# Kernel optimization log

Hardware: AMD Instinct MI355X
Metric: run time of the kernel (lower is better)

Reference implementation:

```python
import jax, jax.numpy as jnp
import numpy as np

B, N, D, H, O = 8, 2048, 64, 64, 64
ALPHA = 2.0  # LeakyReLU negative slope per module default
NEG = -9e15


def _lin(x, W, b):
    # torch nn.Linear: y = x @ W.T + b, W is [out, in]
    return x @ W.T + b


def setup_inputs() -> dict:
    key = jax.random.key(0)
    ks = jax.random.split(key, 32)
    f32 = jnp.float32
    x = jax.random.normal(ks[0], (B, N, D), f32)
    adj = jax.random.randint(ks[1], (B, N, N), 0, 2).astype(f32)
    c = jax.random.normal(ks[2], (B, N, H), f32)
    h = jax.random.normal(ks[3], (B, N, H), f32)
    s = 0.1
    W = jax.random.normal(ks[4], (D, H), f32) * s           # GAT weight
    a = jax.random.normal(ks[5], (2 * H, 1), f32) * s       # GAT attention vector
    def lin(k, out_d, in_d):
        k1, k2 = jax.random.split(k)
        return (jax.random.normal(k1, (out_d, in_d), f32) * s,
                jax.random.normal(k2, (out_d,), f32) * s)
    Wf, bWf = lin(ks[6], H, H); Wi, bWi = lin(ks[7], H, H)
    Wo, bWo = lin(ks[8], H, H); Wc, bWc = lin(ks[9], H, H)
    Uf, bUf = lin(ks[10], H, D); Ui, bUi = lin(ks[11], H, D)
    Uo, bUo = lin(ks[12], H, D); Uc, bUc = lin(ks[13], H, D)
    Wout, bout = lin(ks[14], O, 2 * H)
    return dict(x=x, adj=adj, c=c, h=h, W=W, a=a,
                Wf=Wf, bWf=bWf, Wi=Wi, bWi=bWi, Wo=Wo, bWo=bWo, Wc=Wc, bWc=bWc,
                Uf=Uf, bUf=bUf, Ui=Ui, bUi=bUi, Uo=Uo, bUo=bUo, Uc=Uc, bUc=bUc,
                Wout=Wout, bout=bout)


def reference(x, adj, c, h, W, a,
              Wf, bWf, Wi, bWi, Wo, bWo, Wc, bWc,
              Uf, bUf, Ui, bUi, Uo, bUo, Uc, bUc,
              Wout, bout):
    # ---- GraphAttentionLayer (eval mode: dropout is identity) ----
    Wh = x @ W                                   # [B,N,H]
    # e[b,i,j] = leakyrelu(a[:H].Wh_i + a[H:].Wh_j) -- same math as the
    a_src = (Wh @ a[:H]).squeeze(-1)             # [B,N]
    a_dst = (Wh @ a[H:]).squeeze(-1)             # [B,N]
    e = jax.nn.leaky_relu(a_src[:, :, None] + a_dst[:, None, :], ALPHA)  # [B,N,N]
    att = jnp.where(adj > 0, e, NEG)
    att = jax.nn.softmax(att, axis=2)
    x_hidden = jax.nn.elu(att @ Wh)              # [B,N,H] (concat=True)
    # ---- LSTMLayer step ----
    f_t = jax.nn.sigmoid(_lin(h, Wf, bWf) + _lin(x, Uf, bUf))
    i_t = jax.nn.sigmoid(_lin(h, Wi, bWi) + _lin(x, Ui, bUi))
    o_t = jax.nn.sigmoid(_lin(h, Wo, bWo) + _lin(x, Uo, bUo))
    c_hat = jnp.tanh(_lin(h, Wc, bWc) + _lin(x, Uc, bUc))
    c_t = f_t * c + i_t * c_hat
    h_t = o_t * jax.nn.relu(c_t)                 # gate = nn.ReLU() default
    total = jnp.concatenate([x_hidden, h_t], axis=2)  # [B,N,2H]
    output = jax.nn.relu(_lin(total, Wout, bout))     # [B,N,O]
    return (output, h_t, c_t)
```

## Files before the change

kernel.cpp:

```cpp
#include <hip/hip_runtime.h>
#include <math.h>

#define B_ 8
#define N_ 2048
#define NT_ (B_*N_)
#define OUTSZ (NT_*64)

#define WS_ASRC  0
#define WS_ADST  (WS_ASRC + NT_)
#define WS_EJ    (WS_ADST + NT_)
#define WS_C1    (WS_EJ + NT_)
#define WS_C2    (WS_C1 + NT_)
#define WS_THR   (WS_C2 + NT_)
#define WS_GMAX  (WS_THR + NT_)
#define WS_WT    (WS_GMAX + 32)
#define WS_BB    (WS_WT + 128*256)
#define WS_WOT   (WS_BB + 256)
#define WS_PD    (WS_WOT + 128*64)
#define WS_PN    (WS_PD + 8*NT_)

typedef float f32x4 __attribute__((ext_vector_type(4)));
typedef __bf16 bf16x8 __attribute__((ext_vector_type(8)));
typedef __bf16 bf16x4 __attribute__((ext_vector_type(4)));

__device__ __forceinline__ float lrelu2(float x) { return x > 0.f ? x : 2.f * x; }
__device__ __forceinline__ float f4get(const float4& v, int k) { return k==0?v.x:(k==1?v.y:(k==2?v.z:v.w)); }

__global__ void k0_prep(const float* Wf, const float* Wi, const float* Wo, const float* Wc,
                        const float* Uf, const float* Ui, const float* Uo, const float* Uc,
                        const float* bWf, const float* bWi, const float* bWo, const float* bWc,
                        const float* bUf, const float* bUi, const float* bUo, const float* bUc,
                        const float* Wout, float* ws)
{
    int idx = blockIdx.x * 256 + threadIdx.x;
    if (idx < 128 * 256) {
        int k = idx >> 8, o = idx & 255;
        int g = o >> 6, u = o & 63;
        const float* Wg = (g == 0) ? Wf : (g == 1) ? Wi : (g == 2) ? Wo : Wc;
        const float* Ug = (g == 0) ? Uf : (g == 1) ? Ui : (g == 2) ? Uo : Uc;
        ws[WS_WT + idx] = (k < 64) ? Wg[u * 64 + k] : Ug[u * 64 + (k - 64)];
    } else if (idx < 128 * 256 + 256) {
        int o = idx - 128 * 256;
        int g = o >> 6, u = o & 63;
        const float* bW = (g == 0) ? bWf : (g == 1) ? bWi : (g == 2) ? bWo : bWc;
        const float* bU = (g == 0) ? bUf : (g == 1) ? bUi : (g == 2) ? bUo : bUc;
        ws[WS_BB + o] = bW[u] + bU[u];
    } else if (idx < 128 * 256 + 256 + 128 * 64) {
        int j = idx - (128 * 256 + 256);
        int k = j >> 6, u = j & 63;
        ws[WS_WOT + j] = Wout[u * 128 + k];
    }
}

__global__ __launch_bounds__(256) void k1_wh(const float* __restrict__ x, const float* __restrict__ W,
                                             const float* __restrict__ a, float* __restrict__ ws,
                                             __bf16* __restrict__ whT)
{
    __shared__ float xl[64 * 68];
    __shared__ float Wl[64 * 68];
    int t = threadIdx.x;
    int i0 = blockIdx.x * 64;
    #pragma unroll
    for (int it = 0; it < 4; ++it) {
        int f = t + 256 * it;
        int r = f >> 4, q = f & 15;
        *(float4*)&xl[r * 68 + q * 4] = *(const float4*)&x[i0 * 64 + f * 4];
        *(float4*)&Wl[r * 68 + q * 4] = *(const float4*)&W[f * 4];
    }
    __syncthreads();
    int cg = t & 15, rg = t >> 4;
    int c0 = cg * 4, r0 = rg * 4;
    float acc[4][4] = {};
    #pragma unroll
    for (int d0 = 0; d0 < 64; d0 += 4) {
        float4 wv[4], xv[4];
        #pragma unroll
        for (int k = 0; k < 4; ++k) wv[k] = *(float4*)&Wl[(d0 + k) * 68 + c0];
        #pragma unroll
        for (int ri = 0; ri < 4; ++ri) xv[ri] = *(float4*)&xl[(r0 + ri) * 68 + d0];
        #pragma unroll
        for (int ri = 0; ri < 4; ++ri)
            #pragma unroll
            for (int k = 0; k < 4; ++k) {
                float xs = f4get(xv[ri], k);
                acc[ri][0] += xs * wv[k].x; acc[ri][1] += xs * wv[k].y;
                acc[ri][2] += xs * wv[k].z; acc[ri][3] += xs * wv[k].w;
            }
    }
    int b = i0 >> 11;
    int rowb0 = (i0 & 2047) + r0;
    #pragma unroll
    for (int cj = 0; cj < 4; ++cj) {
        bf16x4 v;
        v[0] = (__bf16)acc[0][cj]; v[1] = (__bf16)acc[1][cj];
        v[2] = (__bf16)acc[2][cj]; v[3] = (__bf16)acc[3][cj];
        *(bf16x4*)&whT[((size_t)(b * 64 + c0 + cj)) * N_ + rowb0] = v;
    }
    float4 a0 = *(const float4*)&a[c0];
    float4 a1 = *(const float4*)&a[64 + c0];
    #pragma unroll
    for (int ri = 0; ri < 4; ++ri) {
        int row = i0 + r0 + ri;
        float s0 = acc[ri][0]*a0.x + acc[ri][1]*a0.y + acc[ri][2]*a0.z + acc[ri][3]*a0.w;
        float s1 = acc[ri][0]*a1.x + acc[ri][1]*a1.y + acc[ri][2]*a1.z + acc[ri][3]*a1.w;
        #pragma unroll
        for (int m = 1; m < 16; m <<= 1) { s0 += __shfl_xor(s0, m, 64); s1 += __shfl_xor(s1, m, 64); }
        if (cg == 0) { ws[WS_ASRC + row] = s0; ws[WS_ADST + row] = s1; }
    }
}

__global__ __launch_bounds__(256) void k1b_prep(float* ws)
{
    __shared__ float red[256];
    __shared__ float gsh;
    int b = blockIdx.x, t = threadIdx.x;
    float m = -3.0e38f;
    for (int j = t; j < N_; j += 256) {
        float v = ws[WS_ADST + b * N_ + j];
        ws[WS_EJ + b * N_ + j] = __expf(v);
        m = fmaxf(m, v);
    }
    red[t] = m; __syncthreads();
    for (int s = 128; s > 0; s >>= 1) { if (t < s) red[t] = fmaxf(red[t], red[t + s]); __syncthreads(); }
    if (t == 0) { gsh = red[0]; ws[WS_GMAX + b] = red[0]; }
    __syncthreads();
    float gmax = gsh;
    for (int i = t; i < N_; i += 256) {
        float as = ws[WS_ASRC + b * N_ + i];
        float M = lrelu2(as + gmax);
        ws[WS_C1 + b * N_ + i]  = __expf(as - M);
        ws[WS_C2 + b * N_ + i]  = __expf(2.f * as - M);
        ws[WS_THR + b * N_ + i] = __expf(-as);
    }
}

__global__ __launch_bounds__(256) void k2v3(const float* __restrict__ adj,
                                            const __bf16* __restrict__ whT,
                                            float* __restrict__ ws)
{
    __shared__ float lsa[4][16][68];
    __shared__ float lsd[4][16];
    int tid = threadIdx.x;
    int lane = tid & 63, w = tid >> 6;
    int r = lane & 15, g = lane >> 4;
    int jr = blockIdx.x & 7;
    int rblk = blockIdx.x >> 3;
    int b = rblk >> 4;
    int row_base = b * N_ + (rblk & 15) * 128;
    int jbeg = jr * 256 + w * 64;

    bf16x8 bfr[2][4];
    #pragma unroll
    for (int ks = 0; ks < 2; ++ks)
        #pragma unroll
        for (int n = 0; n < 4; ++n)
            bfr[ks][n] = *(const bf16x8*)&whT[(size_t)(b * 64 + n * 16 + r) * N_ + jbeg + ks * 32 + g * 8];
    float ejr[2][8];
    #pragma unroll
    for (int ks = 0; ks < 2; ++ks) {
        float4 e0 = *(const float4*)&ws[WS_EJ + b * N_ + jbeg + ks * 32 + g * 8];
        float4 e1 = *(const float4*)&ws[WS_EJ + b * N_ + jbeg + ks * 32 + g * 8 + 4];
        ejr[ks][0]=e0.x; ejr[ks][1]=e0.y; ejr[ks][2]=e0.z; ejr[ks][3]=e0.w;
        ejr[ks][4]=e1.x; ejr[ks][5]=e1.y; ejr[ks][6]=e1.z; ejr[ks][7]=e1.w;
    }

#define LDTILE(T, A0, A1, A2, A3, C1v, C2v, THv)                                   \
    {                                                                              \
        int row0_ = row_base + (T) * 16;                                           \
        const float* ap_ = &adj[(size_t)(row0_ + r) * N_ + jbeg];                  \
        A0 = *(const float4*)&ap_[g * 8];                                          \
        A1 = *(const float4*)&ap_[g * 8 + 4];                                      \
        A2 = *(const float4*)&ap_[32 + g * 8];                                     \
        A3 = *(const float4*)&ap_[32 + g * 8 + 4];                                 \
        C1v = ws[WS_C1 + row0_ + r];                                               \
        C2v = ws[WS_C2 + row0_ + r];                                               \
        THv = ws[WS_THR + row0_ + r];                                              \
    }

    float4 av0, av1, av2, av3; float c1, c2, thr;
    LDTILE(0, av0, av1, av2, av3, c1, c2, thr);

    for (int t = 0; t < 8; ++t) {
        int row0 = row_base + t * 16;
        f32x4 acc[4] = {{0.f,0.f,0.f,0.f},{0.f,0.f,0.f,0.f},{0.f,0.f,0.f,0.f},{0.f,0.f,0.f,0.f}};
        float dsum = 0.f;
        #pragma unroll
        for (int ks = 0; ks < 2; ++ks) {
            bf16x8 af;
            float ds_ = 0.f;
            #pragma unroll
            for (int e = 0; e < 8; ++e) {
                float avv = f4get(e < 4 ? (ks ? av2 : av0) : (ks ? av3 : av1), e & 3);
                float E = ejr[ks][e];
                float p = (E > thr) ? c1 * E : (c2 * E) * E;
                p = (avv > 0.f) ? p : 0.f;
                ds_ += p;
                af[e] = (__bf16)p;
            }
            dsum += ds_;
            #pragma unroll
            for (int n = 0; n < 4; ++n)
                acc[n] = __builtin_amdgcn_mfma_f32_16x16x32_bf16(af, bfr[ks][n], acc[n], 0, 0, 0);
        }
        float4 nv0, nv1, nv2, nv3; float n1, n2, n3;
        if (t < 7) { LDTILE(t + 1, nv0, nv1, nv2, nv3, n1, n2, n3); }
        dsum += __shfl_xor(dsum, 16, 64);
        dsum += __shfl_xor(dsum, 32, 64);
        #pragma unroll
        for (int n = 0; n < 4; ++n)
            #pragma unroll
            for (int i = 0; i < 4; ++i)
                lsa[w][g * 4 + i][n * 16 + r] = acc[n][i];
        if (g == 0) lsd[w][r] = dsum;
        __syncthreads();
        {
            int rl = tid >> 4, h0 = (tid & 15) * 4;
            float4 s = make_float4(0.f, 0.f, 0.f, 0.f);
            #pragma unroll
            for (int w2 = 0; w2 < 4; ++w2) {
                float4 q = *(const float4*)&lsa[w2][rl][h0];
                s.x += q.x; s.y += q.y; s.z += q.z; s.w += q.w;
            }
            *(float4*)&ws[WS_PN + ((size_t)jr * NT_ + row0 + rl) * 64 + h0] = s;
            if (tid < 16)
                ws[WS_PD + jr * NT_ + row0 + tid] = lsd[0][tid] + lsd[1][tid] + lsd[2][tid] + lsd[3][tid];
        }
        __syncthreads();
        av0 = nv0; av1 = nv1; av2 = nv2; av3 = nv3; c1 = n1; c2 = n2; thr = n3;
    }
#undef LDTILE
}

__global__ __launch_bounds__(256) void k3_lstm(const float* __restrict__ x, const float* __restrict__ c,
                                               const float* __restrict__ h, const float* __restrict__ ws,
                                               float* __restrict__ out)
{
    __shared__ float Al[16 * 132];
    __shared__ float gl[16 * 260];
    int t = threadIdx.x;
    int base = blockIdx.x * 16;
    {
        int r = t >> 4, k0 = (t & 15) * 8;
        const float* src = (k0 < 64) ? &h[(base + r) * 64 + k0] : &x[(base + r) * 64 + (k0 - 64)];
        *(float4*)&Al[r * 132 + k0]     = *(const float4*)&src[0];
        *(float4*)&Al[r * 132 + k0 + 4] = *(const float4*)&src[4];
    }
    __syncthreads();
    int og = t & 63, rg = t >> 6;
    int o0 = og * 4;
    const float* WT = &ws[WS_WT];
    float acc[4][4] = {};
    #pragma unroll
    for (int k0 = 0; k0 < 128; k0 += 4) {
        float4 wv[4], av[4];
        #pragma unroll
        for (int kk = 0; kk < 4; ++kk) wv[kk] = *(const float4*)&WT[(k0 + kk) * 256 + o0];
        #pragma unroll
        for (int rr = 0; rr < 4; ++rr) av[rr] = *(float4*)&Al[(rg + 4 * rr) * 132 + k0];
        #pragma unroll
        for (int rr = 0; rr < 4; ++rr)
            #pragma unroll
            for (int kk = 0; kk < 4; ++kk) {
                float as = f4get(av[rr], kk);
                acc[rr][0] += as * wv[kk].x; acc[rr][1] += as * wv[kk].y;
                acc[rr][2] += as * wv[kk].z; acc[rr][3] += as * wv[kk].w;
            }
    }
    float4 bbv = *(const float4*)&ws[WS_BB + o0];
    #pragma unroll
    for (int rr = 0; rr < 4; ++rr) {
        int r = rg + 4 * rr;
        *(float4*)&gl[r * 260 + o0] = make_float4(acc[rr][0] + bbv.x, acc[rr][1] + bbv.y,
                                                  acc[rr][2] + bbv.z, acc[rr][3] + bbv.w);
    }
    __syncthreads();
    int u = t & 63, rq = t >> 6;
    #pragma unroll
    for (int pp = 0; pp < 4; ++pp) {
        int r = rq + 4 * pp;
        float gf = gl[r * 260 + u];
        float gi = gl[r * 260 + 64 + u];
        float go = gl[r * 260 + 128 + u];
        float gc = gl[r * 260 + 192 + u];
        float fg = 1.f / (1.f + __expf(-gf));
        float ig = 1.f / (1.f + __expf(-gi));
        float oo = 1.f / (1.f + __expf(-go));
        float ch = tanhf(gc);
        float cv = c[(base + r) * 64 + u];
        float ct = fg * cv + ig * ch;
        float ht = oo * fmaxf(ct, 0.f);
        out[OUTSZ + (base + r) * 64 + u] = ht;
        out[2 * OUTSZ + (base + r) * 64 + u] = ct;
    }
}

__global__ __launch_bounds__(256) void k5_out(const float* __restrict__ ws, const float* __restrict__ bout,
                                              float* __restrict__ out)
{
    __shared__ float Al[64 * 132];
    int t = threadIdx.x;
    int base = blockIdx.x * 64;
    const float* ht = &out[OUTSZ];
    #pragma unroll
    for (int it = 0; it < 8; ++it) {
        int f = t + 256 * it;
        int r = f >> 5, q = f & 31;
        int k0 = q * 4;
        int row = base + r;
        float4 v;
        if (k0 < 64) {
            float4 s = make_float4(0.f, 0.f, 0.f, 0.f);
            float d = 0.f;
            #pragma unroll
            for (int jr = 0; jr < 8; ++jr) {
                float4 p = *(const float4*)&ws[WS_PN + ((size_t)jr * NT_ + row) * 64 + k0];
                s.x += p.x; s.y += p.y; s.z += p.z; s.w += p.w;
                d += ws[WS_PD + jr * NT_ + row];
            }
            float inv = 1.f / d;
            v.x = s.x * inv; v.x = v.x > 0.f ? v.x : expm1f(v.x);
            v.y = s.y * inv; v.y = v.y > 0.f ? v.y : expm1f(v.y);
            v.z = s.z * inv; v.z = v.z > 0.f ? v.z : expm1f(v.z);
            v.w = s.w * inv; v.w = v.w > 0.f ? v.w : expm1f(v.w);
        } else {
            v = *(const float4*)&ht[(size_t)row * 64 + (k0 - 64)];
        }
        *(float4*)&Al[r * 132 + k0] = v;
    }
    __syncthreads();
    int cg = t & 15, rgG = t >> 4;
    int c0 = cg * 4, r0 = rgG * 4;
    const float* WT = &ws[WS_WOT];
    float acc[4][4] = {};
    #pragma unroll
    for (int k0 = 0; k0 < 128; k0 += 4) {
        float4 wv[4], av[4];
        #pragma unroll
        for (int kk = 0; kk < 4; ++kk) wv[kk] = *(const float4*)&WT[(k0 + kk) * 64 + c0];
        #pragma unroll
        for (int ri = 0; ri < 4; ++ri) av[ri] = *(float4*)&Al[(r0 + ri) * 132 + k0];
        #pragma unroll
        for (int ri = 0; ri < 4; ++ri)
            #pragma unroll
            for (int kk = 0; kk < 4; ++kk) {
                float as = f4get(av[ri], kk);
                acc[ri][0] += as * wv[kk].x; acc[ri][1] += as * wv[kk].y;
                acc[ri][2] += as * wv[kk].z; acc[ri][3] += as * wv[kk].w;
            }
    }
    float4 bo = *(const float4*)&bout[c0];
    #pragma unroll
    for (int ri = 0; ri < 4; ++ri) {
        int row = base + r0 + ri;
        float4 o;
        o.x = fmaxf(acc[ri][0] + bo.x, 0.f);
        o.y = fmaxf(acc[ri][1] + bo.y, 0.f);
        o.z = fmaxf(acc[ri][2] + bo.z, 0.f);
        o.w = fmaxf(acc[ri][3] + bo.w, 0.f);
        *(float4*)&out[row * 64 + c0] = o;
    }
}

extern "C" void kernel_launch(void* const* d_in, const int* in_sizes, int n_in,
                              void* d_out, int out_size, void* d_ws, size_t ws_size,
                              hipStream_t stream)
{
    const float* x    = (const float*)d_in[0];
    const float* adj  = (const float*)d_in[1];
    const float* c    = (const float*)d_in[2];
    const float* h    = (const float*)d_in[3];
    const float* W    = (const float*)d_in[4];
    const float* a    = (const float*)d_in[5];
    const float* Wf   = (const float*)d_in[6];
    const float* bWf  = (const float*)d_in[7];
    const float* Wi   = (const float*)d_in[8];
    const float* bWi  = (const float*)d_in[9];
    const float* Wo   = (const float*)d_in[10];
    const float* bWo  = (const float*)d_in[11];
    const float* Wc   = (const float*)d_in[12];
    const float* bWc  = (const float*)d_in[13];
    const float* Uf   = (const float*)d_in[14];
    const float* bUf  = (const float*)d_in[15];
    const float* Ui   = (const float*)d_in[16];
    const float* bUi  = (const float*)d_in[17];
    const float* Uo   = (const float*)d_in[18];
    const float* bUo  = (const float*)d_in[19];
    const float* Uc   = (const float*)d_in[20];
    const float* bUc  = (const float*)d_in[21];
    const float* Wout = (const float*)d_in[22];
    const float* bout = (const float*)d_in[23];
    float* out = (float*)d_out;
    float* ws  = (float*)d_ws;
    __bf16* whT = (__bf16*)out;

    k0_prep<<<161, 256, 0, stream>>>(Wf, Wi, Wo, Wc, Uf, Ui, Uo, Uc,
                                     bWf, bWi, bWo, bWc, bUf, bUi, bUo, bUc, Wout, ws);
    k1_wh<<<NT_ / 64, 256, 0, stream>>>(x, W, a, ws, whT);
    k1b_prep<<<B_, 256, 0, stream>>>(ws);
    k3_lstm<<<NT_ / 16, 256, 0, stream>>>(x, c, h, ws, out);
    k2v3<<<1024, 256, 0, stream>>>(adj, whT, ws);
    k5_out<<<NT_ / 64, 256, 0, stream>>>(ws, bout, out);
}
```

Before: 99.58 us.

## Fuse weight prep into Wh kernel and restructure attention kernel with deeper prefetch

The weight-transpose prep kernel is folded into extra blocks of the Wh kernel, removing one launch. The attention/aggregation kernel now uses 512-thread blocks covering 512 columns each, which halves the number of column partials written and later summed by the output kernel. It also prefetches adj tiles two steps ahead with a 3-slot register ring and double-buffers the shared reduction buffers, replacing two full syncthreads with a single barrier per tile. The trade-offs are higher register pressure from the unrolled ring buffer and only half the threads working during the reduction phase.

```diff
diff --git a/kernel.cpp b/kernel.cpp
--- a/kernel.cpp
+++ b/kernel.cpp
@@ -17,7 +17,7 @@
 #define WS_BB    (WS_WT + 128*256)
 #define WS_WOT   (WS_BB + 256)
 #define WS_PD    (WS_WOT + 128*64)
-#define WS_PN    (WS_PD + 8*NT_)
+#define WS_PN    (WS_PD + 4*NT_)
 
 typedef float f32x4 __attribute__((ext_vector_type(4)));
 typedef __bf16 bf16x8 __attribute__((ext_vector_type(8)));
@@ -26,39 +26,39 @@
 __device__ __forceinline__ float lrelu2(float x) { return x > 0.f ? x : 2.f * x; }
 __device__ __forceinline__ float f4get(const float4& v, int k) { return k==0?v.x:(k==1?v.y:(k==2?v.z:v.w)); }
 
-__global__ void k0_prep(const float* Wf, const float* Wi, const float* Wo, const float* Wc,
-                        const float* Uf, const float* Ui, const float* Uo, const float* Uc,
-                        const float* bWf, const float* bWi, const float* bWo, const float* bWc,
-                        const float* bUf, const float* bUi, const float* bUo, const float* bUc,
-                        const float* Wout, float* ws)
-{
-    int idx = blockIdx.x * 256 + threadIdx.x;
-    if (idx < 128 * 256) {
-        int k = idx >> 8, o = idx & 255;
-        int g = o >> 6, u = o & 63;
-        const float* Wg = (g == 0) ? Wf : (g == 1) ? Wi : (g == 2) ? Wo : Wc;
-        const float* Ug = (g == 0) ? Uf : (g == 1) ? Ui : (g == 2) ? Uo : Uc;
-        ws[WS_WT + idx] = (k < 64) ? Wg[u * 64 + k] : Ug[u * 64 + (k - 64)];
-    } else if (idx < 128 * 256 + 256) {
-        int o = idx - 128 * 256;
-        int g = o >> 6, u = o & 63;
-        const float* bW = (g == 0) ? bWf : (g == 1) ? bWi : (g == 2) ? bWo : bWc;
-        const float* bU = (g == 0) ? bUf : (g == 1) ? bUi : (g == 2) ? bUo : bUc;
-        ws[WS_BB + o] = bW[u] + bU[u];
-    } else if (idx < 128 * 256 + 256 + 128 * 64) {
-        int j = idx - (128 * 256 + 256);
-        int k = j >> 6, u = j & 63;
-        ws[WS_WOT + j] = Wout[u * 128 + k];
-    }
-}
-
 __global__ __launch_bounds__(256) void k1_wh(const float* __restrict__ x, const float* __restrict__ W,
                                              const float* __restrict__ a, float* __restrict__ ws,
-                                             __bf16* __restrict__ whT)
+                                             __bf16* __restrict__ whT,
+                                             const float* Wf, const float* Wi, const float* Wo, const float* Wc,
+                                             const float* Uf, const float* Ui, const float* Uo, const float* Uc,
+                                             const float* bWf, const float* bWi, const float* bWo, const float* bWc,
+                                             const float* bUf, const float* bUi, const float* bUo, const float* bUc,
+                                             const float* Wout)
 {
     __shared__ float xl[64 * 68];
     __shared__ float Wl[64 * 68];
     int t = threadIdx.x;
+    if (blockIdx.x >= 256) {
+        int idx = (blockIdx.x - 256) * 256 + t;
+        if (idx < 128 * 256) {
+            int k = idx >> 8, o = idx & 255;
+            int g = o >> 6, u = o & 63;
+            const float* Wg = (g == 0) ? Wf : (g == 1) ? Wi : (g == 2) ? Wo : Wc;
+            const float* Ug = (g == 0) ? Uf : (g == 1) ? Ui : (g == 2) ? Uo : Uc;
+            ws[WS_WT + idx] = (k < 64) ? Wg[u * 64 + k] : Ug[u * 64 + (k - 64)];
+        } else if (idx < 128 * 256 + 256) {
+            int o = idx - 128 * 256;
+            int g = o >> 6, u = o & 63;
+            const float* bW = (g == 0) ? bWf : (g == 1) ? bWi : (g == 2) ? bWo : bWc;
+            const float* bU = (g == 0) ? bUf : (g == 1) ? bUi : (g == 2) ? bUo : bUc;
+            ws[WS_BB + o] = bW[u] + bU[u];
+        } else if (idx < 128 * 256 + 256 + 128 * 64) {
+            int j = idx - (128 * 256 + 256);
+            int k = j >> 6, u = j & 63;
+            ws[WS_WOT + j] = Wout[u * 128 + k];
+        }
+        return;
+    }
     int i0 = blockIdx.x * 64;
     #pragma unroll
     for (int it = 0; it < 4; ++it) {
@@ -134,20 +134,20 @@
     }
 }
 
-__global__ __launch_bounds__(256) void k2v3(const float* __restrict__ adj,
-                                            const __bf16* __restrict__ whT,
-                                            float* __restrict__ ws)
-{
-    __shared__ float lsa[4][16][68];
-    __shared__ float lsd[4][16];
+__global__ __launch_bounds__(512, 4) void k2v4(const float* __restrict__ adj,
+                                               const __bf16* __restrict__ whT,
+                                               float* __restrict__ ws)
+{
+    __shared__ float lsa[2][8][16][68];
+    __shared__ float lsd[2][8][16];
     int tid = threadIdx.x;
     int lane = tid & 63, w = tid >> 6;
     int r = lane & 15, g = lane >> 4;
-    int jr = blockIdx.x & 7;
-    int rblk = blockIdx.x >> 3;
-    int b = rblk >> 4;
-    int row_base = b * N_ + (rblk & 15) * 128;
-    int jbeg = jr * 256 + w * 64;
+    int jr = blockIdx.x & 3;
+    int rslab = blockIdx.x >> 2;
+    int b = rslab >> 4;
+    int row_base = rslab * 128;
+    int jbeg = jr * 512 + w * 64;
 
     bf16x8 bfr[2][4];
     #pragma unroll
@@ -164,33 +164,39 @@
         ejr[ks][4]=e1.x; ejr[ks][5]=e1.y; ejr[ks][6]=e1.z; ejr[ks][7]=e1.w;
     }
 
-#define LDTILE(T, A0, A1, A2, A3, C1v, C2v, THv)                                   \
+    float4 av[3][4];
+    float c1v[3], c2v[3], thv[3];
+
+#define LDT(T, S)                                                                  \
     {                                                                              \
         int row0_ = row_base + (T) * 16;                                           \
         const float* ap_ = &adj[(size_t)(row0_ + r) * N_ + jbeg];                  \
-        A0 = *(const float4*)&ap_[g * 8];                                          \
-        A1 = *(const float4*)&ap_[g * 8 + 4];                                      \
-        A2 = *(const float4*)&ap_[32 + g * 8];                                     \
-        A3 = *(const float4*)&ap_[32 + g * 8 + 4];                                 \
-        C1v = ws[WS_C1 + row0_ + r];                                               \
-        C2v = ws[WS_C2 + row0_ + r];                                               \
-        THv = ws[WS_THR + row0_ + r];                                              \
-    }
-
-    float4 av0, av1, av2, av3; float c1, c2, thr;
-    LDTILE(0, av0, av1, av2, av3, c1, c2, thr);
-
+        av[S][0] = *(const float4*)&ap_[g * 8];                                    \
+        av[S][1] = *(const float4*)&ap_[g * 8 + 4];                                \
+        av[S][2] = *(const float4*)&ap_[32 + g * 8];                               \
+        av[S][3] = *(const float4*)&ap_[32 + g * 8 + 4];                           \
+        c1v[S] = ws[WS_C1 + row0_ + r];                                            \
+        c2v[S] = ws[WS_C2 + row0_ + r];                                            \
+        thv[S] = ws[WS_THR + row0_ + r];                                           \
+    }
+
+    LDT(0, 0);
+    LDT(1, 1);
+
+    #pragma unroll
     for (int t = 0; t < 8; ++t) {
-        int row0 = row_base + t * 16;
+        const int s = t % 3;
+        if (t + 2 < 8) { LDT(t + 2, (t + 2) % 3); }
         f32x4 acc[4] = {{0.f,0.f,0.f,0.f},{0.f,0.f,0.f,0.f},{0.f,0.f,0.f,0.f},{0.f,0.f,0.f,0.f}};
         float dsum = 0.f;
+        float c1 = c1v[s], c2 = c2v[s], thr = thv[s];
         #pragma unroll
         for (int ks = 0; ks < 2; ++ks) {
             bf16x8 af;
             float ds_ = 0.f;
             #pragma unroll
             for (int e = 0; e < 8; ++e) {
-                float avv = f4get(e < 4 ? (ks ? av2 : av0) : (ks ? av3 : av1), e & 3);
+                float avv = f4get(e < 4 ? av[s][ks * 2] : av[s][ks * 2 + 1], e & 3);
                 float E = ejr[ks][e];
                 float p = (E > thr) ? c1 * E : (c2 * E) * E;
                 p = (avv > 0.f) ? p : 0.f;
@@ -202,33 +208,36 @@
             for (int n = 0; n < 4; ++n)
                 acc[n] = __builtin_amdgcn_mfma_f32_16x16x32_bf16(af, bfr[ks][n], acc[n], 0, 0, 0);
         }
-        float4 nv0, nv1, nv2, nv3; float n1, n2, n3;
-        if (t < 7) { LDTILE(t + 1, nv0, nv1, nv2, nv3, n1, n2, n3); }
         dsum += __shfl_xor(dsum, 16, 64);
         dsum += __shfl_xor(dsum, 32, 64);
         #pragma unroll
         for (int n = 0; n < 4; ++n)
             #pragma unroll
             for (int i = 0; i < 4; ++i)
-                lsa[w][g * 4 + i][n * 16 + r] = acc[n][i];
-        if (g == 0) lsd[w][r] = dsum;
-        __syncthreads();
-        {
+                lsa[t & 1][w][g * 4 + i][n * 16 + r] = acc[n][i];
+        if (g == 0) lsd[t & 1][w][r] = dsum;
+        asm volatile("s_waitcnt lgkmcnt(0)" ::: "memory");
+        __builtin_amdgcn_s_barrier();
+        asm volatile("" ::: "memory");
+        if (tid < 256) {
             int rl = tid >> 4, h0 = (tid & 15) * 4;
-            float4 s = make_float4(0.f, 0.f, 0.f, 0.f);
-            #pragma unroll
-            for (int w2 = 0; w2 < 4; ++w2) {
-                float4 q = *(const float4*)&lsa[w2][rl][h0];
-                s.x += q.x; s.y += q.y; s.z += q.z; s.w += q.w;
-            }
-            *(float4*)&ws[WS_PN + ((size_t)jr * NT_ + row0 + rl) * 64 + h0] = s;
-            if (tid < 16)
-                ws[WS_PD + jr * NT_ + row0 + tid] = lsd[0][tid] + lsd[1][tid] + lsd[2][tid] + lsd[3][tid];
+            float4 sv = make_float4(0.f, 0.f, 0.f, 0.f);
+            #pragma unroll
+            for (int w2 = 0; w2 < 8; ++w2) {
+                float4 q = *(const float4*)&lsa[t & 1][w2][rl][h0];
+                sv.x += q.x; sv.y += q.y; sv.z += q.z; sv.w += q.w;
+            }
+            int row0 = row_base + t * 16;
+            *(float4*)&ws[WS_PN + ((size_t)jr * NT_ + row0 + rl) * 64 + h0] = sv;
+            if (tid < 16) {
+                float d = 0.f;
+                #pragma unroll
+                for (int w2 = 0; w2 < 8; ++w2) d += lsd[t & 1][w2][tid];
+                ws[WS_PD + jr * NT_ + row0 + tid] = d;
+            }
         }
-        __syncthreads();
-        av0 = nv0; av1 = nv1; av2 = nv2; av3 = nv3; c1 = n1; c2 = n2; thr = n3;
-    }
-#undef LDTILE
+    }
+#undef LDT
 }
 
 __global__ __launch_bounds__(256) void k3_lstm(const float* __restrict__ x, const float* __restrict__ c,
@@ -312,7 +321,7 @@
             float4 s = make_float4(0.f, 0.f, 0.f, 0.f);
             float d = 0.f;
             #pragma unroll
-            for (int jr = 0; jr < 8; ++jr) {
+            for (int jr = 0; jr < 4; ++jr) {
                 float4 p = *(const float4*)&ws[WS_PN + ((size_t)jr * NT_ + row) * 64 + k0];
                 s.x += p.x; s.y += p.y; s.z += p.z; s.w += p.w;
                 d += ws[WS_PD + jr * NT_ + row];
@@ -393,11 +402,11 @@
     float* ws  = (float*)d_ws;
     __bf16* whT = (__bf16*)out;
 
-    k0_prep<<<161, 256, 0, stream>>>(Wf, Wi, Wo, Wc, Uf, Ui, Uo, Uc,
-                                     bWf, bWi, bWo, bWc, bUf, bUi, bUo, bUc, Wout, ws);
-    k1_wh<<<NT_ / 64, 256, 0, stream>>>(x, W, a, ws, whT);
+    k1_wh<<<417, 256, 0, stream>>>(x, W, a, ws, whT,
+                                   Wf, Wi, Wo, Wc, Uf, Ui, Uo, Uc,
+                                   bWf, bWi, bWo, bWc, bUf, bUi, bUo, bUc, Wout);
     k1b_prep<<<B_, 256, 0, stream>>>(ws);
     k3_lstm<<<NT_ / 16, 256, 0, stream>>>(x, c, h, ws, out);
-    k2v3<<<1024, 256, 0, stream>>>(adj, whT, ws);
+    k2v4<<<512, 512, 0, stream>>>(adj, whT, ws);
     k5_out<<<NT_ / 64, 256, 0, stream>>>(ws, bout, out);
 }
```

New measurement: 106.7 us. 1.07x slower.
